# Kernel optimization log

Hardware: AMD Instinct MI355X
Metric: run time of the kernel (lower is better)

Reference implementation:

```python
import jax, jax.numpy as jnp
import numpy as np


def setup_inputs() -> dict:
    key = jax.random.key(0)
    kq, kk, kv, km = jax.random.split(key, 4)
    B, H, S, D = 2, 16, 2048, 64
    Q = jax.random.normal(kq, (B, H, S, D), dtype=jnp.float32)
    K = jax.random.normal(kk, (B, H, S, D), dtype=jnp.float32)
    V = jax.random.normal(kv, (B, H, S, D), dtype=jnp.float32)
    mask = jax.random.randint(km, (B, 1, S, S), 0, 2).astype(jnp.bool_)
    return {"Q": Q, "K": K, "V": V, "mask": mask}


def reference(Q, K, V, mask):
    # scores: [B, H, Sq, Sk]
    scores = jnp.einsum("bhqd,bhkd->bhqk", Q, K)
    neg = jnp.finfo(scores.dtype).min
    # Faithful to original: mask fill happens BEFORE the sqrt(d) scaling.
    scores = jnp.where(mask, neg, scores)
    inv_sqrt_d = 1.0 / jnp.sqrt(jnp.asarray(Q.shape[-1], dtype=scores.dtype))
    attn = jax.nn.softmax(scores * inv_sqrt_d, axis=-1)
    return jnp.einsum("bhqk,bhkd->bhqd", attn, V)
```

## Files before the change

kernel.cpp:

```cpp
#include <hip/hip_runtime.h>
#include <stdint.h>


#define SQ 2048
#define DH 64

using bf16x8  = __attribute__((ext_vector_type(8)))  __bf16;
using f32x16  = __attribute__((ext_vector_type(16))) float;
using ushort8 = __attribute__((ext_vector_type(8)))  unsigned short;
using ushort4v= __attribute__((ext_vector_type(4)))  unsigned short;

static __device__ __forceinline__ unsigned short f2bf(float f) {
    union { float f; uint32_t u; } c; c.f = f;
    return (unsigned short)((c.u + 0x8000u) >> 16);
}

static __device__ __forceinline__ int swz(int row, int col) {
    return row * 64 + ((((col >> 3) ^ (row & 7))) << 3) + (col & 7);
}

static __device__ __forceinline__ f32x16 mfma(bf16x8 a, bf16x8 b, f32x16 c) {
    return __builtin_amdgcn_mfma_f32_32x32x16_bf16(a, b, c, 0, 0, 0);
}

__global__ void pack_mask_kernel(const int* __restrict__ mask,
                                 unsigned long long* __restrict__ words, int nwords) {
    int gid = blockIdx.x * blockDim.x + threadIdx.x;
    int w = gid >> 6;
    int l = gid & 63;
    if (w < nwords) {
        int mv = mask[(size_t)w * 64 + l];
        unsigned long long b = __ballot(mv != 0);
        if (l == 0) words[w] = b;
    }
}

__global__ __launch_bounds__(256, 2)
void attn_kernel(const float* __restrict__ Q, const float* __restrict__ K,
                 const float* __restrict__ V,
                 const unsigned long long* __restrict__ Mw,
                 float* __restrict__ out) {
    __shared__ __align__(16) unsigned short Ks[64 * 64];
    __shared__ __align__(16) unsigned short Vt[64 * 64];
    __shared__ __align__(16) unsigned short Ps[4 * 32 * 64];

    const int tid = threadIdx.x;
    const int w = tid >> 6;
    const int l = tid & 63;
    const int m = l & 31;
    const int h = l >> 5;
    const unsigned bitm = 1u << m;
    const int bx = blockIdx.x;
    const int hh = bx & 15;
    const int b  = (bx >> 4) & 1;
    const int qt = bx >> 5;

    const size_t bh = (size_t)b * 16 + hh;
    const float* Qp = Q + bh * SQ * DH;
    const float* Kp = K + bh * SQ * DH;
    const float* Vp = V + bh * SQ * DH;
    const int qw = qt * 128 + 32 * w;
    const unsigned long long* Mb = Mw + ((size_t)b * SQ + qw) * (SQ / 64);

    bf16x8 qf[4];
    {
        const float* qr = Qp + (size_t)(qw + m) * DH;
        #pragma unroll
        for (int c = 0; c < 4; ++c) {
            int d0 = 16 * c + 8 * h;
            float4 a  = *(const float4*)(qr + d0);
            float4 bb = *(const float4*)(qr + d0 + 4);
            ushort8 t;
            t[0]=f2bf(a.x);  t[1]=f2bf(a.y);  t[2]=f2bf(a.z);  t[3]=f2bf(a.w);
            t[4]=f2bf(bb.x); t[5]=f2bf(bb.y); t[6]=f2bf(bb.z); t[7]=f2bf(bb.w);
            qf[c] = __builtin_bit_cast(bf16x8, t);
        }
    }

    f32x16 o0, o1;
    float lsum[16];
    #pragma unroll
    for (int i = 0; i < 16; ++i) { o0[i] = 0.f; o1[i] = 0.f; lsum[i] = 0.f; }

    unsigned short* Pw = Ps + w * (32 * 64);

    for (int kt0 = 0; kt0 < SQ; kt0 += 64) {
        unsigned long long mws[16];
        {
            const unsigned long long* mwp = Mb + (kt0 >> 6);
            #pragma unroll
            for (int r = 0; r < 16; ++r) {
                int row = (r & 3) + 8 * (r >> 2) + 4 * h;
                mws[r] = mwp[(size_t)row * (SQ / 64)];
            }
        }

        __syncthreads();

        #pragma unroll
        for (int i = 0; i < 4; ++i) {
            int idx = tid + 256 * i;
            int key = idx >> 4;
            int d0  = (idx & 15) << 2;
            float4 kv = *(const float4*)(Kp + (size_t)(kt0 + key) * DH + d0);
            ushort4v t;
            t[0]=f2bf(kv.x); t[1]=f2bf(kv.y); t[2]=f2bf(kv.z); t[3]=f2bf(kv.w);
            *(ushort4v*)&Ks[swz(key, d0)] = t;
        }
        #pragma unroll
        for (int p = 0; p < 4; ++p) {
            int k0l = 16 * w + 4 * p;
            const float* vb = Vp + (size_t)(kt0 + k0l) * DH + l;
            float x0 = vb[0], x1 = vb[DH], x2 = vb[2*DH], x3 = vb[3*DH];
            ushort4v t;
            t[0]=f2bf(x0); t[1]=f2bf(x1); t[2]=f2bf(x2); t[3]=f2bf(x3);
            *(ushort4v*)&Vt[swz(l, k0l)] = t;
        }
        __syncthreads();

        f32x16 s0, s1;
        #pragma unroll
        for (int i = 0; i < 16; ++i) { s0[i] = 0.f; s1[i] = 0.f; }
        #pragma unroll
        for (int c = 0; c < 4; ++c) {
            int g = ((2 * c + h) ^ (l & 7)) << 3;
            bf16x8 kb0 = __builtin_bit_cast(bf16x8, *(const ushort8*)&Ks[m * 64 + g]);
            bf16x8 kb1 = __builtin_bit_cast(bf16x8, *(const ushort8*)&Ks[(32 + m) * 64 + g]);
            s0 = mfma(qf[c], kb0, s0);
            s1 = mfma(qf[c], kb1, s1);
        }

        #pragma unroll
        for (int r = 0; r < 16; ++r) {
            int row = (r & 3) + 8 * (r >> 2) + 4 * h;
            unsigned lo = (unsigned)mws[r];
            unsigned hi = (unsigned)(mws[r] >> 32);
            float e0 = exp2f(fmaf(s0[r], 0.18033688f, -5.7707802f));
            float e1 = exp2f(fmaf(s1[r], 0.18033688f, -5.7707802f));
            float p0 = (lo & bitm) ? 0.0f : e0;
            float p1 = (hi & bitm) ? 0.0f : e1;
            lsum[r] += p0 + p1;
            Pw[swz(row, m)]      = f2bf(p0);
            Pw[swz(row, 32 + m)] = f2bf(p1);
        }

        #pragma unroll
        for (int c = 0; c < 4; ++c) {
            int g = ((2 * c + h) ^ (l & 7)) << 3;
            bf16x8 pa  = __builtin_bit_cast(bf16x8, *(const ushort8*)&Pw[m * 64 + g]);
            bf16x8 vb0 = __builtin_bit_cast(bf16x8, *(const ushort8*)&Vt[m * 64 + g]);
            bf16x8 vb1 = __builtin_bit_cast(bf16x8, *(const ushort8*)&Vt[(32 + m) * 64 + g]);
            o0 = mfma(pa, vb0, o0);
            o1 = mfma(pa, vb1, o1);
        }
    }

    #pragma unroll
    for (int r = 0; r < 16; ++r) {
        float v = lsum[r];
        v += __shfl_xor(v, 1, 64);
        v += __shfl_xor(v, 2, 64);
        v += __shfl_xor(v, 4, 64);
        v += __shfl_xor(v, 8, 64);
        v += __shfl_xor(v, 16, 64);
        float rinv = 1.0f / v;
        int row = (r & 3) + 8 * (r >> 2) + 4 * h;
        float* op = out + (bh * SQ + (size_t)(qw + row)) * DH;
        op[m]      = o0[r] * rinv;
        op[32 + m] = o1[r] * rinv;
    }
}

extern "C" void kernel_launch(void* const* d_in, const int* in_sizes, int n_in,
                              void* d_out, int out_size, void* d_ws, size_t ws_size,
                              hipStream_t stream) {
    const float* Q    = (const float*)d_in[0];
    const float* K    = (const float*)d_in[1];
    const float* V    = (const float*)d_in[2];
    const int*   mask = (const int*)d_in[3];
    float* out = (float*)d_out;
    unsigned long long* mwords = (unsigned long long*)d_ws;

    const int nwords = 2 * SQ * (SQ / 64);
    pack_mask_kernel<<<dim3((nwords * 64) / 256), dim3(256), 0, stream>>>(mask, mwords, nwords);
    attn_kernel<<<dim3(512), dim3(256), 0, stream>>>(Q, K, V, mwords, out);
}
```

Before: 208.6 us.

## Split key dimension across two blocks with atomic accumulation and normalize pass

Splits the key sequence into two halves, doubling the grid to 1024 blocks so more CUs are occupied. Each block accumulates its unnormalized partial output and row sums into global memory with atomicAdd, then a separate kernel divides by the sums. This is valid because the kernel uses a fixed max offset rather than a running max, so partial results add directly. It adds two memsets, atomic traffic and an extra kernel launch in exchange for more parallelism.

```diff
diff --git a/kernel.cpp b/kernel.cpp
--- a/kernel.cpp
+++ b/kernel.cpp
@@ -39,7 +39,7 @@
 void attn_kernel(const float* __restrict__ Q, const float* __restrict__ K,
                  const float* __restrict__ V,
                  const unsigned long long* __restrict__ Mw,
-                 float* __restrict__ out) {
+                 float* __restrict__ outNum, float* __restrict__ sums) {
     __shared__ __align__(16) unsigned short Ks[64 * 64];
     __shared__ __align__(16) unsigned short Vt[64 * 64];
     __shared__ __align__(16) unsigned short Ps[4 * 32 * 64];
@@ -53,7 +53,8 @@
     const int bx = blockIdx.x;
     const int hh = bx & 15;
     const int b  = (bx >> 4) & 1;
-    const int qt = bx >> 5;
+    const int qt = (bx >> 5) & 15;
+    const int ks = bx >> 9;
 
     const size_t bh = (size_t)b * 16 + hh;
     const float* Qp = Q + bh * SQ * DH;
@@ -84,7 +85,9 @@
 
     unsigned short* Pw = Ps + w * (32 * 64);
 
-    for (int kt0 = 0; kt0 < SQ; kt0 += 64) {
+    for (int t = 0; t < 16; ++t) {
+        const int kt0 = ks * 1024 + t * 64;
+
         unsigned long long mws[16];
         {
             const unsigned long long* mwp = Mb + (kt0 >> 6);
@@ -103,18 +106,18 @@
             int key = idx >> 4;
             int d0  = (idx & 15) << 2;
             float4 kv = *(const float4*)(Kp + (size_t)(kt0 + key) * DH + d0);
-            ushort4v t;
-            t[0]=f2bf(kv.x); t[1]=f2bf(kv.y); t[2]=f2bf(kv.z); t[3]=f2bf(kv.w);
-            *(ushort4v*)&Ks[swz(key, d0)] = t;
+            ushort4v tt;
+            tt[0]=f2bf(kv.x); tt[1]=f2bf(kv.y); tt[2]=f2bf(kv.z); tt[3]=f2bf(kv.w);
+            *(ushort4v*)&Ks[swz(key, d0)] = tt;
         }
         #pragma unroll
         for (int p = 0; p < 4; ++p) {
             int k0l = 16 * w + 4 * p;
             const float* vb = Vp + (size_t)(kt0 + k0l) * DH + l;
             float x0 = vb[0], x1 = vb[DH], x2 = vb[2*DH], x3 = vb[3*DH];
-            ushort4v t;
-            t[0]=f2bf(x0); t[1]=f2bf(x1); t[2]=f2bf(x2); t[3]=f2bf(x3);
-            *(ushort4v*)&Vt[swz(l, k0l)] = t;
+            ushort4v tt;
+            tt[0]=f2bf(x0); tt[1]=f2bf(x1); tt[2]=f2bf(x2); tt[3]=f2bf(x3);
+            *(ushort4v*)&Vt[swz(l, k0l)] = tt;
         }
         __syncthreads();
 
@@ -163,12 +166,22 @@
         v += __shfl_xor(v, 4, 64);
         v += __shfl_xor(v, 8, 64);
         v += __shfl_xor(v, 16, 64);
-        float rinv = 1.0f / v;
         int row = (r & 3) + 8 * (r >> 2) + 4 * h;
-        float* op = out + (bh * SQ + (size_t)(qw + row)) * DH;
-        op[m]      = o0[r] * rinv;
-        op[32 + m] = o1[r] * rinv;
-    }
+        float* op = outNum + (bh * SQ + (size_t)(qw + row)) * DH;
+        atomicAdd(&op[m],      o0[r]);
+        atomicAdd(&op[32 + m], o1[r]);
+        if (m == 0) atomicAdd(&sums[bh * SQ + (size_t)(qw + row)], v);
+    }
+}
+
+__global__ __launch_bounds__(256)
+void normalize_kernel(float* __restrict__ out, const float* __restrict__ sums) {
+    int gid = blockIdx.x * 256 + threadIdx.x;
+    float rinv = 1.0f / sums[gid >> 4];
+    float4* o4 = (float4*)out;
+    float4 v = o4[gid];
+    v.x *= rinv; v.y *= rinv; v.z *= rinv; v.w *= rinv;
+    o4[gid] = v;
 }
 
 extern "C" void kernel_launch(void* const* d_in, const int* in_sizes, int n_in,
@@ -180,8 +193,12 @@
     const int*   mask = (const int*)d_in[3];
     float* out = (float*)d_out;
     unsigned long long* mwords = (unsigned long long*)d_ws;
+    float* sums = (float*)((char*)d_ws + (1 << 20));
 
     const int nwords = 2 * SQ * (SQ / 64);
+    hipMemsetAsync(d_out, 0, (size_t)out_size * sizeof(float), stream);
+    hipMemsetAsync(sums, 0, 32 * SQ * sizeof(float), stream);
     pack_mask_kernel<<<dim3((nwords * 64) / 256), dim3(256), 0, stream>>>(mask, mwords, nwords);
-    attn_kernel<<<dim3(512), dim3(256), 0, stream>>>(Q, K, V, mwords, out);
-}
+    attn_kernel<<<dim3(1024), dim3(256), 0, stream>>>(Q, K, V, mwords, out, sums);
+    normalize_kernel<<<dim3(out_size / (4 * 256)), dim3(256), 0, stream>>>(out, sums);
+}
```

New measurement: 241.4 us. 15.7% more time.
